# Performance work log

Measured on AMD Instinct MI355X. Metric: run time of the kernel, lower is better.

Reference implementation:

```python
import jax, jax.numpy as jnp
import numpy as np

ALPHA = 0.25
GAMMA = 2.0
PROB_MIN = 0.0001


def _gather_feat(feat, inds):
    # feat: [B, C, H, W], inds: [B, K] in [0, H*W) -> [B, K, C]
    B, C, H, W = feat.shape
    f = feat.reshape(B, C, H * W).transpose(0, 2, 1)  # [B, HW, C]
    return jnp.take_along_axis(f, inds[:, :, None], axis=1)


def setup_inputs() -> dict:
    key = jax.random.key(0)
    ks = jax.random.split(key, 7)
    B, C, H, W, K = 8, 64, 152, 272, 500
    HW = H * W
    cur_reid = jax.random.normal(ks[0], (B, C, H, W), dtype=jnp.float32)
    pre_reid = jax.random.normal(ks[1], (B, C, H, W), dtype=jnp.float32)
    cur_inds = jax.random.randint(ks[2], (B, K), 0, HW, dtype=jnp.int64)
    pre_inds = jax.random.randint(ks[3], (B, K), 0, HW, dtype=jnp.int64)
    cur_circum_ind = jax.random.randint(ks[4], (B, K), 0, HW, dtype=jnp.int64)
    pre_circum_ind = jax.random.randint(ks[5], (B, K), 0, HW, dtype=jnp.int64)
    tracking_mask = jax.random.randint(ks[6], (B, K, 1), 0, 2, dtype=jnp.int32)
    return {
        "cur_reid": cur_reid,
        "pre_reid": pre_reid,
        "cur_inds": cur_inds,
        "pre_inds": pre_inds,
        "cur_circum_ind": cur_circum_ind,
        "pre_circum_ind": pre_circum_ind,
        "tracking_mask": tracking_mask,
    }


def reference(cur_reid, pre_reid, cur_inds, pre_inds, cur_circum_ind, pre_circum_ind, tracking_mask):
    mask = tracking_mask[:, :, 0].astype(jnp.int64)  # [B, K], 0/1
    # Replace indices of non-tracked slots with the pre-drawn random indices
    cur_idx = cur_inds * mask + cur_circum_ind * (1 - mask)
    pre_idx = pre_inds * mask + pre_circum_ind * (1 - mask)

    cur_feat = _gather_feat(cur_reid, cur_idx)  # [B, K, C]
    pre_feat = _gather_feat(pre_reid, pre_idx)  # [B, K, C]

    # similarity[b, i, j] = sigmoid(<cur_feat[b,i], pre_feat[b,j]>)
    sim = jax.nn.sigmoid(jnp.einsum("bic,bjc->bij", cur_feat, pre_feat))  # [B, K, K]

    # groundtruth = diag_embed(mask): gt[b,i,i] = mask[b,i]
    K = mask.shape[1]
    gt = mask[:, :, None] * jnp.eye(K, dtype=mask.dtype)[None]  # [B, K, K]

    # focal loss: p_t = sim if gt==1 else 1-sim; alpha_t = 0.25 if gt==1 else 0.75
    probs = jnp.where(gt == 1, sim, 1.0 - sim)
    probs = jnp.clip(probs, PROB_MIN, 1.0)
    alpha_t = jnp.where(gt == 1, ALPHA, 1.0 - ALPHA)
    loss = jnp.mean(-alpha_t * (1.0 - probs) ** GAMMA * jnp.log(probs))
    return loss
```

## Files before the change

kernel.cpp:

```cpp
#include <hip/hip_runtime.h>

#define B 8
#define C 64
#define H 152
#define W 272
#define HW (H * W)
#define K 500
#define KP 512
#define ALPHA 0.25f
#define PROB_MIN 1e-4f

typedef __attribute__((ext_vector_type(8))) short short8;
typedef __attribute__((ext_vector_type(4))) float floatx4;

__device__ __forceinline__ unsigned short f32_to_bf16(float f) {
    union { float f; unsigned int u; } v; v.f = f;
    unsigned int r = v.u + 0x7FFFu + ((v.u >> 16) & 1u);
    return (unsigned short)(r >> 16);
}

__global__ __launch_bounds__(256) void gather_kernel(
    const float* __restrict__ cur_reid,
    const float* __restrict__ pre_reid,
    const int* __restrict__ cur_inds,
    const int* __restrict__ pre_inds,
    const int* __restrict__ cur_circ,
    const int* __restrict__ pre_circ,
    const int* __restrict__ tmask,
    unsigned short* __restrict__ curf,
    unsigned short* __restrict__ pref,
    float* __restrict__ out)
{
    const int c   = blockIdx.x;
    const int b   = blockIdx.y;
    const int arr = blockIdx.z;
    const int t   = threadIdx.x;

    if (c == 0 && b == 0 && arr == 0 && t == 0)
        out[0] = 0.0f;

    const float* plane = (arr ? pre_reid : cur_reid) + ((size_t)(b * C + c)) * HW;
    const int* inds = arr ? pre_inds : cur_inds;
    const int* circ = arr ? pre_circ : cur_circ;
    unsigned short* feat = arr ? pref : curf;

#pragma unroll
    for (int r = 0; r < 2; ++r) {
        const int k = t + r * 256;
        unsigned short v = 0;
        if (k < K) {
            const int bk  = b * K + k;
            const int idx = tmask[bk] ? inds[bk] : circ[bk];
            v = f32_to_bf16(plane[idx]);
        }
        feat[((size_t)(b * KP + k)) * C + c] = v;
    }
}

__device__ __forceinline__ float focal_term(float x, int gi, int gj, int b,
                                            const int* __restrict__ tmask)
{
    if (gi >= K || gj >= K) return 0.0f;
    const float sim = 1.0f / (1.0f + __expf(-x));
    const int gt = (gi == gj) ? tmask[b * K + gi] : 0;
    float p = gt ? sim : 1.0f - sim;
    p = fminf(fmaxf(p, PROB_MIN), 1.0f);
    const float a = gt ? ALPHA : (1.0f - ALPHA);
    const float om = 1.0f - p;
    return a * om * om * (-__logf(p));
}

#define LOSS_THREADS 1024

__global__ __launch_bounds__(LOSS_THREADS) void loss_kernel(
    const unsigned short* __restrict__ curf,
    const unsigned short* __restrict__ pref,
    const int* __restrict__ tmask,
    float* __restrict__ out)
{
    __shared__ float wsum[LOSS_THREADS / 64];

    const int t    = threadIdx.x;
    const int wave = t >> 6;
    const int lane = t & 63;

    const int tile = blockIdx.x * (LOSS_THREADS / 64) + wave;
    const int b    = tile >> 10;
    const int rem  = tile & 1023;
    const int ti   = rem >> 5;
    const int tj   = rem & 31;

    const int m16  = lane & 15;
    const int quad = lane >> 4;

    const unsigned short* pa = curf + (((size_t)(b * KP + ti * 16 + m16)) * C + quad * 8);
    const unsigned short* pb = pref + (((size_t)(b * KP + tj * 16 + m16)) * C + quad * 8);
    const short8 a0 = *(const short8*)pa;
    const short8 a1 = *(const short8*)(pa + 32);
    const short8 b0 = *(const short8*)pb;
    const short8 b1 = *(const short8*)(pb + 32);

    floatx4 acc = {0.f, 0.f, 0.f, 0.f};
    acc = __builtin_amdgcn_mfma_f32_16x16x32_bf16(a0, b0, acc, 0, 0, 0);
    acc = __builtin_amdgcn_mfma_f32_16x16x32_bf16(a1, b1, acc, 0, 0, 0);

    const int gj = tj * 16 + m16;
    float s = 0.f;
#pragma unroll
    for (int r = 0; r < 4; ++r) {
        const int gi = ti * 16 + quad * 4 + r;
        s += focal_term(acc[r], gi, gj, b, tmask);
    }

#pragma unroll
    for (int o = 32; o > 0; o >>= 1) s += __shfl_down(s, o, 64);
    if (lane == 0) wsum[wave] = s;
    __syncthreads();
    if (t == 0) {
        float tot = 0.f;
#pragma unroll
        for (int w = 0; w < LOSS_THREADS / 64; ++w) tot += wsum[w];
        atomicAdd(out, tot * (1.0f / ((float)B * (float)K * (float)K)));
    }
}

extern "C" void kernel_launch(void* const* d_in, const int* in_sizes, int n_in,
                              void* d_out, int out_size, void* d_ws, size_t ws_size,
                              hipStream_t stream)
{
    const float* cur_reid = (const float*)d_in[0];
    const float* pre_reid = (const float*)d_in[1];
    const int*   cur_inds = (const int*)d_in[2];
    const int*   pre_inds = (const int*)d_in[3];
    const int*   cur_circ = (const int*)d_in[4];
    const int*   pre_circ = (const int*)d_in[5];
    const int*   tmask    = (const int*)d_in[6];
    float*       out      = (float*)d_out;

    unsigned short* curf = (unsigned short*)d_ws;
    unsigned short* pref = curf + (size_t)B * KP * C;

    dim3 ggrid(C, B, 2);
    gather_kernel<<<ggrid, 256, 0, stream>>>(
        cur_reid, pre_reid, cur_inds, pre_inds, cur_circ, pre_circ, tmask,
        curf, pref, out);

    loss_kernel<<<512, LOSS_THREADS, 0, stream>>>(curf, pref, tmask, out);
}
```

Before: 180.5 us.

## Fuse gather and focal-loss kernels into one cooperative kernel with grid sync

Replaces the separate gather and loss launches with a single cooperative kernel. All 256 blocks first gather the cur and pre features to bf16, then wait at a grid-wide barrier, then compute the MFMA similarity tiles and focal loss. Each wave now handles two tiles instead of one. This removes one kernel launch and the gap between kernels. In exchange it adds a grid sync, depends on cooperative-launch overhead, and halves the number of blocks in the loss phase.

```diff
diff --git a/kernel.cpp b/kernel.cpp
--- a/kernel.cpp
+++ b/kernel.cpp
@@ -1,4 +1,7 @@
 #include <hip/hip_runtime.h>
+#include <hip/hip_cooperative_groups.h>
+
+namespace cg = cooperative_groups;
 
 #define B 8
 #define C 64
@@ -10,6 +13,9 @@
 #define ALPHA 0.25f
 #define PROB_MIN 1e-4f
 
+#define NBLK 256
+#define NTHR 1024
+
 typedef __attribute__((ext_vector_type(8))) short short8;
 typedef __attribute__((ext_vector_type(4))) float floatx4;
 
@@ -17,44 +23,6 @@
     union { float f; unsigned int u; } v; v.f = f;
     unsigned int r = v.u + 0x7FFFu + ((v.u >> 16) & 1u);
     return (unsigned short)(r >> 16);
-}
-
-__global__ __launch_bounds__(256) void gather_kernel(
-    const float* __restrict__ cur_reid,
-    const float* __restrict__ pre_reid,
-    const int* __restrict__ cur_inds,
-    const int* __restrict__ pre_inds,
-    const int* __restrict__ cur_circ,
-    const int* __restrict__ pre_circ,
-    const int* __restrict__ tmask,
-    unsigned short* __restrict__ curf,
-    unsigned short* __restrict__ pref,
-    float* __restrict__ out)
-{
-    const int c   = blockIdx.x;
-    const int b   = blockIdx.y;
-    const int arr = blockIdx.z;
-    const int t   = threadIdx.x;
-
-    if (c == 0 && b == 0 && arr == 0 && t == 0)
-        out[0] = 0.0f;
-
-    const float* plane = (arr ? pre_reid : cur_reid) + ((size_t)(b * C + c)) * HW;
-    const int* inds = arr ? pre_inds : cur_inds;
-    const int* circ = arr ? pre_circ : cur_circ;
-    unsigned short* feat = arr ? pref : curf;
-
-#pragma unroll
-    for (int r = 0; r < 2; ++r) {
-        const int k = t + r * 256;
-        unsigned short v = 0;
-        if (k < K) {
-            const int bk  = b * K + k;
-            const int idx = tmask[bk] ? inds[bk] : circ[bk];
-            v = f32_to_bf16(plane[idx]);
-        }
-        feat[((size_t)(b * KP + k)) * C + c] = v;
-    }
 }
 
 __device__ __forceinline__ float focal_term(float x, int gi, int gj, int b,
@@ -70,48 +38,78 @@
     return a * om * om * (-__logf(p));
 }
 
-#define LOSS_THREADS 1024
-
-__global__ __launch_bounds__(LOSS_THREADS) void loss_kernel(
-    const unsigned short* __restrict__ curf,
-    const unsigned short* __restrict__ pref,
+__global__ __launch_bounds__(NTHR, 4) void fused_kernel(
+    const float* __restrict__ cur_reid,
+    const float* __restrict__ pre_reid,
+    const int* __restrict__ cur_inds,
+    const int* __restrict__ pre_inds,
+    const int* __restrict__ cur_circ,
+    const int* __restrict__ pre_circ,
     const int* __restrict__ tmask,
+    unsigned short* __restrict__ curf,
+    unsigned short* __restrict__ pref,
     float* __restrict__ out)
 {
-    __shared__ float wsum[LOSS_THREADS / 64];
+    const int t   = threadIdx.x;
+    const int tid = blockIdx.x * NTHR + t;
 
-    const int t    = threadIdx.x;
+    if (tid == 0) out[0] = 0.0f;
+    {
+        const int c = tid & 63;
+        const int k = (tid >> 6) & (KP - 1);
+        const int b = tid >> 15;
+        unsigned short vc = 0, vp = 0;
+        if (k < K) {
+            const int bk = b * K + k;
+            const int m  = tmask[bk];
+            const int ic = m ? cur_inds[bk] : cur_circ[bk];
+            const int ip = m ? pre_inds[bk] : pre_circ[bk];
+            const size_t plane = ((size_t)(b * C + c)) * HW;
+            vc = f32_to_bf16(cur_reid[plane + ic]);
+            vp = f32_to_bf16(pre_reid[plane + ip]);
+        }
+        const size_t o = ((size_t)(b * KP + k)) * C + c;
+        curf[o] = vc;
+        pref[o] = vp;
+    }
+
+    __threadfence();
+    cg::this_grid().sync();
+
     const int wave = t >> 6;
     const int lane = t & 63;
-
-    const int tile = blockIdx.x * (LOSS_THREADS / 64) + wave;
-    const int b    = tile >> 10;
-    const int rem  = tile & 1023;
-    const int ti   = rem >> 5;
-    const int tj   = rem & 31;
-
     const int m16  = lane & 15;
     const int quad = lane >> 4;
+    const int w0   = blockIdx.x * (NTHR / 64) + wave;
 
-    const unsigned short* pa = curf + (((size_t)(b * KP + ti * 16 + m16)) * C + quad * 8);
-    const unsigned short* pb = pref + (((size_t)(b * KP + tj * 16 + m16)) * C + quad * 8);
-    const short8 a0 = *(const short8*)pa;
-    const short8 a1 = *(const short8*)(pa + 32);
-    const short8 b0 = *(const short8*)pb;
-    const short8 b1 = *(const short8*)(pb + 32);
-
-    floatx4 acc = {0.f, 0.f, 0.f, 0.f};
-    acc = __builtin_amdgcn_mfma_f32_16x16x32_bf16(a0, b0, acc, 0, 0, 0);
-    acc = __builtin_amdgcn_mfma_f32_16x16x32_bf16(a1, b1, acc, 0, 0, 0);
-
-    const int gj = tj * 16 + m16;
     float s = 0.f;
 #pragma unroll
-    for (int r = 0; r < 4; ++r) {
-        const int gi = ti * 16 + quad * 4 + r;
-        s += focal_term(acc[r], gi, gj, b, tmask);
+    for (int rep = 0; rep < 2; ++rep) {
+        const int tile = w0 + rep * 4096;
+        const int b  = tile >> 10;
+        const int ti = (tile >> 5) & 31;
+        const int tj = tile & 31;
+
+        const unsigned short* pa = curf + (((size_t)(b * KP + ti * 16 + m16)) * C + quad * 8);
+        const unsigned short* pb = pref + (((size_t)(b * KP + tj * 16 + m16)) * C + quad * 8);
+        const short8 a0 = *(const short8*)pa;
+        const short8 a1 = *(const short8*)(pa + 32);
+        const short8 b0 = *(const short8*)pb;
+        const short8 b1 = *(const short8*)(pb + 32);
+
+        floatx4 acc = {0.f, 0.f, 0.f, 0.f};
+        acc = __builtin_amdgcn_mfma_f32_16x16x32_bf16(a0, b0, acc, 0, 0, 0);
+        acc = __builtin_amdgcn_mfma_f32_16x16x32_bf16(a1, b1, acc, 0, 0, 0);
+
+        const int gj = tj * 16 + m16;
+#pragma unroll
+        for (int r = 0; r < 4; ++r) {
+            const int gi = ti * 16 + quad * 4 + r;
+            s += focal_term(acc[r], gi, gj, b, tmask);
+        }
     }
 
+    __shared__ float wsum[NTHR / 64];
 #pragma unroll
     for (int o = 32; o > 0; o >>= 1) s += __shfl_down(s, o, 64);
     if (lane == 0) wsum[wave] = s;
@@ -119,7 +117,7 @@
     if (t == 0) {
         float tot = 0.f;
 #pragma unroll
-        for (int w = 0; w < LOSS_THREADS / 64; ++w) tot += wsum[w];
+        for (int w = 0; w < NTHR / 64; ++w) tot += wsum[w];
         atomicAdd(out, tot * (1.0f / ((float)B * (float)K * (float)K)));
     }
 }
@@ -140,10 +138,12 @@
     unsigned short* curf = (unsigned short*)d_ws;
     unsigned short* pref = curf + (size_t)B * KP * C;
 
-    dim3 ggrid(C, B, 2);
-    gather_kernel<<<ggrid, 256, 0, stream>>>(
-        cur_reid, pre_reid, cur_inds, pre_inds, cur_circ, pre_circ, tmask,
-        curf, pref, out);
-
-    loss_kernel<<<512, LOSS_THREADS, 0, stream>>>(curf, pref, tmask, out);
+    void* args[] = {
+        (void*)&cur_reid, (void*)&pre_reid,
+        (void*)&cur_inds, (void*)&pre_inds,
+        (void*)&cur_circ, (void*)&pre_circ,
+        (void*)&tmask, (void*)&curf, (void*)&pref, (void*)&out
+    };
+    hipLaunchCooperativeKernel((const void*)fused_kernel,
+                               dim3(NBLK), dim3(NTHR), args, 0, stream);
 }
```

Result: slower. 362.7 us (+101.0%).
